# Optimization experiments

Measured on AMD Instinct MI355X. Metric: run time of the kernel, lower is better.

Reference implementation:

```python
import jax, jax.numpy as jnp
import numpy as np

B, C, W, H, D = 2, 256, 32, 32, 32
CH = C // 2  # 128
LN_EPS = 1e-5


def _spatial_pool(x, wm, bm):
    # x: [B,C,W,H,D]; wm: [C]; bm: scalar. 1x1x1 conv C->1 == channel dot.
    b, c = x.shape[0], x.shape[1]
    xf = x.reshape(b, c, -1)                       # [B,C,N]
    mask = jnp.einsum('bcn,c->bn', xf, wm) + bm    # [B,N]
    attn = jax.nn.softmax(mask, axis=1)            # softmax over spatial N
    return jnp.einsum('bcn,bn->bc', xf, attn)      # [B,C] weighted-sum pool


def _channel_add(ctx, w1, b1, g, be, w2, b2):
    # 1x1 conv C->C/2, LayerNorm over C/2, ReLU, 1x1 conv C/2->C
    h = ctx @ w1.T + b1                            # [B,CH]
    mu = jnp.mean(h, axis=-1, keepdims=True)
    var = jnp.mean((h - mu) ** 2, axis=-1, keepdims=True)
    h = (h - mu) * jax.lax.rsqrt(var + LN_EPS) * g + be
    h = jax.nn.relu(h)
    return h @ w2.T + b2                           # [B,C]


def setup_inputs() -> dict:
    key = jax.random.key(0)
    ks = jax.random.split(key, 20)
    s = 0.02
    d = {
        'preds_S': jax.random.normal(ks[0], (B, C, W, H, D), jnp.float32),
        'preds_T': jax.random.normal(ks[1], (B, C, W, H, D), jnp.float32),
        'wm_s': jax.random.normal(ks[2], (C,), jnp.float32) * s,
        'bm_s': jnp.zeros((), jnp.float32),
        'wm_t': jax.random.normal(ks[3], (C,), jnp.float32) * s,
        'bm_t': jnp.zeros((), jnp.float32),
        'w1_s': jax.random.normal(ks[4], (CH, C), jnp.float32) * s,
        'b1_s': jnp.zeros((CH,), jnp.float32),
        'g_s': jnp.ones((CH,), jnp.float32),
        'be_s': jnp.zeros((CH,), jnp.float32),
        'w2_s': jax.random.normal(ks[5], (C, CH), jnp.float32) * s,
        'b2_s': jnp.zeros((C,), jnp.float32),
        'w1_t': jax.random.normal(ks[6], (CH, C), jnp.float32) * s,
        'b1_t': jnp.zeros((CH,), jnp.float32),
        'g_t': jnp.ones((CH,), jnp.float32),
        'be_t': jnp.zeros((CH,), jnp.float32),
        'w2_t': jax.random.normal(ks[7], (C, CH), jnp.float32) * s,
        'b2_t': jnp.zeros((C,), jnp.float32),
    }
    return d


def reference(preds_S, preds_T, wm_s, bm_s, wm_t, bm_t,
              w1_s, b1_s, g_s, be_s, w2_s, b2_s,
              w1_t, b1_t, g_t, be_t, w2_t, b2_t):
    ctx_s = _spatial_pool(preds_S, wm_s, bm_s)     # [B,C]
    ctx_t = _spatial_pool(preds_T, wm_t, bm_t)
    add_s = _channel_add(ctx_s, w1_s, b1_s, g_s, be_s, w2_s, b2_s)  # [B,C]
    add_t = _channel_add(ctx_t, w1_t, b1_t, g_t, be_t, w2_t, b2_t)
    out_s = preds_S + add_s[:, :, None, None, None]
    out_t = preds_T + add_t[:, :, None, None, None]
    diff = out_s - out_t
    return jnp.sum(diff * diff) / preds_S.shape[0]
```

## Files before the change

kernel.cpp:

```cpp
#include <hip/hip_runtime.h>
#include <math.h>

#define Bc   2
#define Cc   256
#define Nn   32768
#define CHc  128
#define LN_EPS 1e-5f

#define TN    64
#define TPB   512
#define NQ    16
#define CG    32
#define CPG   8
#define GRIDX (Nn / TN)
#define NSLOT 16

__global__ __launch_bounds__(TPB, 2) void gc_fused(
    const float* __restrict__ S, const float* __restrict__ T,
    const float* __restrict__ wms, const float* __restrict__ bms,
    const float* __restrict__ wmt, const float* __restrict__ bmt,
    float* __restrict__ ctxnum,
    float* __restrict__ rowsum,
    float* __restrict__ den,
    float* __restrict__ sumsq) {
  const int b    = blockIdx.y;
  const int tid  = threadIdx.x;
  const int nq   = tid & (NQ - 1);
  const int cg   = tid >> 4;
  const int wv   = tid >> 6;
  const int lane = tid & 63;
  const int c0   = cg * CPG;
  const int n0   = blockIdx.x * TN + nq * 4;
  const int slot = blockIdx.x & (NSLOT - 1);

  __shared__ float4 mredw[2][8][NQ];
  __shared__ float  cred[Cc * 17];
  __shared__ float  sqred[8];
  __shared__ float  denred[2][NQ];

  const float bS = bms[0];
  const float bT = bmt[0];

  const float* Sp = S + ((size_t)b * Cc + c0) * Nn + n0;
  const float* Tp = T + ((size_t)b * Cc + c0) * Nn + n0;

  float4 s4[CPG], t4[CPG];
#pragma unroll
  for (int i = 0; i < CPG; ++i) s4[i] = *(const float4*)(Sp + (size_t)i * Nn);
#pragma unroll
  for (int i = 0; i < CPG; ++i) t4[i] = *(const float4*)(Tp + (size_t)i * Nn);

  float wS[CPG], wT[CPG];
#pragma unroll
  for (int i = 0; i < CPG; ++i) { wS[i] = wms[c0 + i]; wT[i] = wmt[c0 + i]; }

  float4 ms = make_float4(0.f, 0.f, 0.f, 0.f);
  float4 mt = make_float4(0.f, 0.f, 0.f, 0.f);
#pragma unroll
  for (int i = 0; i < CPG; ++i) {
    ms.x += wS[i] * s4[i].x; ms.y += wS[i] * s4[i].y;
    ms.z += wS[i] * s4[i].z; ms.w += wS[i] * s4[i].w;
    mt.x += wT[i] * t4[i].x; mt.y += wT[i] * t4[i].y;
    mt.z += wT[i] * t4[i].z; mt.w += wT[i] * t4[i].w;
  }

#pragma unroll
  for (int m = 16; m <= 32; m <<= 1) {
    ms.x += __shfl_xor(ms.x, m); ms.y += __shfl_xor(ms.y, m);
    ms.z += __shfl_xor(ms.z, m); ms.w += __shfl_xor(ms.w, m);
    mt.x += __shfl_xor(mt.x, m); mt.y += __shfl_xor(mt.y, m);
    mt.z += __shfl_xor(mt.z, m); mt.w += __shfl_xor(mt.w, m);
  }
  if (lane < NQ) { mredw[0][wv][nq] = ms; mredw[1][wv][nq] = mt; }

  __syncthreads();

  float4 Ms = make_float4(0.f, 0.f, 0.f, 0.f);
  float4 Mt = make_float4(0.f, 0.f, 0.f, 0.f);
#pragma unroll
  for (int w = 0; w < 8; ++w) {
    const float4 a = mredw[0][w][nq];
    Ms.x += a.x; Ms.y += a.y; Ms.z += a.z; Ms.w += a.w;
    const float4 c = mredw[1][w][nq];
    Mt.x += c.x; Mt.y += c.y; Mt.z += c.z; Mt.w += c.w;
  }
  float4 es, et;
  es.x = __expf(Ms.x + bS); es.y = __expf(Ms.y + bS);
  es.z = __expf(Ms.z + bS); es.w = __expf(Ms.w + bS);
  et.x = __expf(Mt.x + bT); et.y = __expf(Mt.y + bT);
  et.z = __expf(Mt.z + bT); et.w = __expf(Mt.w + bT);

  if (tid < NQ) {
    denred[0][tid] = es.x + es.y + es.z + es.w;
    denred[1][tid] = et.x + et.y + et.z + et.w;
  }

#pragma unroll
  for (int i = 0; i < CPG; ++i)
    cred[(c0 + i) * 17 + nq] =
        s4[i].x * es.x + s4[i].y * es.y + s4[i].z * es.z + s4[i].w * es.w;
  __syncthreads();
  if (tid < Cc) {
    float a = 0.f;
#pragma unroll
    for (int k = 0; k < NQ; ++k) a += cred[tid * 17 + k];
    atomicAdd(&ctxnum[(((size_t)slot * 2 + 0) * Bc + b) * Cc + tid], a);
  } else if (tid == Cc + 1) {
    float a = 0.f, c = 0.f;
#pragma unroll
    for (int k = 0; k < NQ; ++k) { a += denred[0][k]; c += denred[1][k]; }
    atomicAdd(&den[slot * 4 + 0 * Bc + b], a);
    atomicAdd(&den[slot * 4 + 1 * Bc + b], c);
  }
  __syncthreads();

#pragma unroll
  for (int i = 0; i < CPG; ++i)
    cred[(c0 + i) * 17 + nq] =
        t4[i].x * et.x + t4[i].y * et.y + t4[i].z * et.z + t4[i].w * et.w;
  __syncthreads();
  if (tid < Cc) {
    float c = 0.f;
#pragma unroll
    for (int k = 0; k < NQ; ++k) c += cred[tid * 17 + k];
    atomicAdd(&ctxnum[(((size_t)slot * 2 + 1) * Bc + b) * Cc + tid], c);
  }
  __syncthreads();

  float sq = 0.f;
#pragma unroll
  for (int i = 0; i < CPG; ++i) {
    const float dx = s4[i].x - t4[i].x, dy = s4[i].y - t4[i].y;
    const float dz = s4[i].z - t4[i].z, dw = s4[i].w - t4[i].w;
    cred[(c0 + i) * 17 + nq] = dx + dy + dz + dw;
    sq += dx * dx + dy * dy + dz * dz + dw * dw;
  }
#pragma unroll
  for (int m = 1; m < 64; m <<= 1) sq += __shfl_xor(sq, m);
  if (lane == 0) sqred[wv] = sq;
  __syncthreads();
  if (tid < Cc) {
    float r = 0.f;
#pragma unroll
    for (int k = 0; k < NQ; ++k) r += cred[tid * 17 + k];
    atomicAdd(&rowsum[((size_t)slot * Bc + b) * Cc + tid], r);
  } else if (tid == Cc) {
    float v = 0.f;
#pragma unroll
    for (int w = 0; w < 8; ++w) v += sqred[w];
    atomicAdd(&sumsq[slot], v);
  }
}

__global__ __launch_bounds__(1024) void gc_k4a_mlp(
    const float* __restrict__ ctxr, const float* __restrict__ den,
    const float* __restrict__ w1s, const float* __restrict__ b1s,
    const float* __restrict__ gs,  const float* __restrict__ bes,
    const float* __restrict__ w2s, const float* __restrict__ b2s,
    const float* __restrict__ w1t, const float* __restrict__ b1t,
    const float* __restrict__ gt,  const float* __restrict__ bet,
    const float* __restrict__ w2t, const float* __restrict__ b2t,
    float* __restrict__ addv) {
  const int tt  = blockIdx.x >> 1;
  const int b   = blockIdx.x & 1;
  const int tid = threadIdx.x;

  const float* w1 = tt ? w1t : w1s;
  const float* b1 = tt ? b1t : b1s;
  const float* g  = tt ? gt  : gs;
  const float* be = tt ? bet : bes;
  const float* w2 = tt ? w2t : w2s;
  const float* b2 = tt ? b2t : b2s;

  __shared__ float cxs[Cc];
  __shared__ float part[1024];
  __shared__ float hbuf[CHc];
  __shared__ float hr[CHc];
  __shared__ float2 red2[128];
  __shared__ float mu_s, rstd_s;

  if (tid < Cc) {
    float num = 0.f, dn = 0.f;
#pragma unroll
    for (int k = 0; k < NSLOT; ++k) {
      num += ctxr[(((size_t)k * 2 + tt) * Bc + b) * Cc + tid];
      dn  += den[k * 4 + tt * Bc + b];
    }
    cxs[tid] = num / dn;
  }
  __syncthreads();

  {
    const int j = tid >> 3, s = tid & 7;
    const float* wr = w1 + j * Cc + s * 32;
    const float4* cx4 = (const float4*)(cxs + s * 32);
    float acc = 0.f;
#pragma unroll
    for (int k = 0; k < 8; ++k) {
      const float4 w = *(const float4*)(wr + k * 4);
      const float4 x = cx4[k];
      acc += w.x * x.x + w.y * x.y + w.z * x.z + w.w * x.w;
    }
    part[tid] = acc;
  }
  __syncthreads();
  if (tid < CHc) {
    float h = b1[tid];
#pragma unroll
    for (int q = 0; q < 8; ++q) h += part[tid * 8 + q];
    hbuf[tid] = h;
  }
  __syncthreads();

  if (tid < CHc) {
    const float v = hbuf[tid];
    red2[tid] = make_float2(v, v * v);
  }
  __syncthreads();
  for (int s = 64; s > 0; s >>= 1) {
    if (tid < s) {
      red2[tid].x += red2[tid + s].x;
      red2[tid].y += red2[tid + s].y;
    }
    __syncthreads();
  }
  if (tid == 0) {
    const float mu = red2[0].x / (float)CHc;
    const float var = red2[0].y / (float)CHc - mu * mu;
    mu_s = mu;
    rstd_s = rsqrtf(var + LN_EPS);
  }
  __syncthreads();
  if (tid < CHc) {
    const float v = (hbuf[tid] - mu_s) * rstd_s * g[tid] + be[tid];
    hr[tid] = v > 0.f ? v : 0.f;
  }
  __syncthreads();

  {
    const int c = tid >> 2, q = tid & 3;
    const float* wr = w2 + c * CHc + q * 32;
    const float4* h4 = (const float4*)(hr + q * 32);
    float acc = 0.f;
#pragma unroll
    for (int k = 0; k < 8; ++k) {
      const float4 w = *(const float4*)(wr + k * 4);
      const float4 x = h4[k];
      acc += w.x * x.x + w.y * x.y + w.z * x.z + w.w * x.w;
    }
    part[tid] = acc;
  }
  __syncthreads();
  if (tid < Cc) {
    float acc = b2[tid];
#pragma unroll
    for (int q = 0; q < 4; ++q) acc += part[tid * 4 + q];
    addv[((size_t)tt * Bc + b) * Cc + tid] = acc;
  }
}

__global__ __launch_bounds__(256) void gc_k4b_final(
    const float* __restrict__ addv, const float* __restrict__ rowsum,
    const float* __restrict__ sumsq, float* __restrict__ out) {
  const int tid = threadIdx.x;
  __shared__ float red[256];
  float part = 0.f;
  for (int job = tid; job < Bc * Cc; job += 256) {
    const int c = job & (Cc - 1);
    const int b = job >> 8;
    const float delta = addv[((size_t)0 * Bc + b) * Cc + c] -
                        addv[((size_t)1 * Bc + b) * Cc + c];
    float rs = 0.f;
#pragma unroll
    for (int k = 0; k < NSLOT; ++k)
      rs += rowsum[((size_t)k * Bc + b) * Cc + c];
    part += 2.f * delta * rs + (float)Nn * delta * delta;
  }
  red[tid] = part;
  __syncthreads();
  for (int s = 128; s > 0; s >>= 1) {
    if (tid < s) red[tid] += red[tid + s];
    __syncthreads();
  }
  if (tid == 0) {
    float sq = 0.f;
#pragma unroll
    for (int k = 0; k < NSLOT; ++k) sq += sumsq[k];
    out[0] = (red[0] + sq) / (float)Bc;
  }
}

extern "C" void kernel_launch(void* const* d_in, const int* in_sizes, int n_in,
                              void* d_out, int out_size, void* d_ws,
                              size_t ws_size, hipStream_t stream) {
  const float* S   = (const float*)d_in[0];
  const float* T   = (const float*)d_in[1];
  const float* wms = (const float*)d_in[2];
  const float* bms = (const float*)d_in[3];
  const float* wmt = (const float*)d_in[4];
  const float* bmt = (const float*)d_in[5];
  const float* w1s = (const float*)d_in[6];
  const float* b1s = (const float*)d_in[7];
  const float* gs  = (const float*)d_in[8];
  const float* bes = (const float*)d_in[9];
  const float* w2s = (const float*)d_in[10];
  const float* b2s = (const float*)d_in[11];
  const float* w1t = (const float*)d_in[12];
  const float* b1t = (const float*)d_in[13];
  const float* gt  = (const float*)d_in[14];
  const float* bet = (const float*)d_in[15];
  const float* w2t = (const float*)d_in[16];
  const float* b2t = (const float*)d_in[17];
  float* out = (float*)d_out;

  float* ws     = (float*)d_ws;
  float* ctxnum = ws;
  float* rowsum = ctxnum + NSLOT * 2 * Bc * Cc;
  float* den    = rowsum + NSLOT * Bc * Cc;
  float* sumsq  = den + NSLOT * 4;
  float* addv   = sumsq + NSLOT;

  hipMemsetAsync(d_ws, 0,
                 (NSLOT * (2 * Bc * Cc + Bc * Cc + 4 + 1)) * sizeof(float),
                 stream);

  gc_fused<<<dim3(GRIDX, Bc), TPB, 0, stream>>>(S, T, wms, bms, wmt, bmt,
                                                ctxnum, rowsum, den, sumsq);
  gc_k4a_mlp<<<4, 1024, 0, stream>>>(ctxnum, den, w1s, b1s, gs, bes, w2s, b2s,
                                     w1t, b1t, gt, bet, w2t, b2t, addv);
  gc_k4b_final<<<1, 256, 0, stream>>>(addv, rowsum, sumsq, out);
}
```

Before: 195.8 us.

## Replace LDS channel reductions with wave shuffles and widen atomic slots

The per-channel partial sums for the student context, teacher context and S−T rowsum are now reduced with 16-lane xor shuffles in registers. Each lane then picks one channel's value and issues the global atomic itself, instead of staging through a padded shared-memory array. This removes the cred/denred shared buffers and several block-wide barriers, which should shorten the critical path and lower LDS use. The number of atomic slots is doubled to spread contention. The cost is more shuffle instructions and register pressure, and more slots for the MLP kernel to sum.

Result: no change. 192.6 us (-1.7%).

```diff
diff --git a/kernel.cpp b/kernel.cpp
--- a/kernel.cpp
+++ b/kernel.cpp
@@ -13,7 +13,7 @@
 #define CG    32
 #define CPG   8
 #define GRIDX (Nn / TN)
-#define NSLOT 16
+#define NSLOT 32
 
 __global__ __launch_bounds__(TPB, 2) void gc_fused(
     const float* __restrict__ S, const float* __restrict__ T,
@@ -29,14 +29,13 @@
   const int cg   = tid >> 4;
   const int wv   = tid >> 6;
   const int lane = tid & 63;
+  const int sub  = lane & 15;
   const int c0   = cg * CPG;
   const int n0   = blockIdx.x * TN + nq * 4;
   const int slot = blockIdx.x & (NSLOT - 1);
 
   __shared__ float4 mredw[2][8][NQ];
-  __shared__ float  cred[Cc * 17];
   __shared__ float  sqred[8];
-  __shared__ float  denred[2][NQ];
 
   const float bS = bms[0];
   const float bT = bmt[0];
@@ -73,6 +72,24 @@
   }
   if (lane < NQ) { mredw[0][wv][nq] = ms; mredw[1][wv][nq] = mt; }
 
+  float pd[CPG];
+  float sq = 0.f;
+#pragma unroll
+  for (int i = 0; i < CPG; ++i) {
+    const float dx = s4[i].x - t4[i].x, dy = s4[i].y - t4[i].y;
+    const float dz = s4[i].z - t4[i].z, dw = s4[i].w - t4[i].w;
+    pd[i] = dx + dy + dz + dw;
+    sq += dx * dx + dy * dy + dz * dz + dw * dw;
+  }
+#pragma unroll
+  for (int m = 1; m <= 8; m <<= 1) {
+#pragma unroll
+    for (int i = 0; i < CPG; ++i) pd[i] += __shfl_xor(pd[i], m);
+  }
+#pragma unroll
+  for (int m = 1; m < 64; m <<= 1) sq += __shfl_xor(sq, m);
+  if (lane == 0) sqred[wv] = sq;
+
   __syncthreads();
 
   float4 Ms = make_float4(0.f, 0.f, 0.f, 0.f);
@@ -90,61 +107,46 @@
   et.x = __expf(Mt.x + bT); et.y = __expf(Mt.y + bT);
   et.z = __expf(Mt.z + bT); et.w = __expf(Mt.w + bT);
 
-  if (tid < NQ) {
-    denred[0][tid] = es.x + es.y + es.z + es.w;
-    denred[1][tid] = et.x + et.y + et.z + et.w;
-  }
-
-#pragma unroll
-  for (int i = 0; i < CPG; ++i)
-    cred[(c0 + i) * 17 + nq] =
-        s4[i].x * es.x + s4[i].y * es.y + s4[i].z * es.z + s4[i].w * es.w;
-  __syncthreads();
-  if (tid < Cc) {
-    float a = 0.f;
-#pragma unroll
-    for (int k = 0; k < NQ; ++k) a += cred[tid * 17 + k];
-    atomicAdd(&ctxnum[(((size_t)slot * 2 + 0) * Bc + b) * Cc + tid], a);
-  } else if (tid == Cc + 1) {
-    float a = 0.f, c = 0.f;
-#pragma unroll
-    for (int k = 0; k < NQ; ++k) { a += denred[0][k]; c += denred[1][k]; }
-    atomicAdd(&den[slot * 4 + 0 * Bc + b], a);
-    atomicAdd(&den[slot * 4 + 1 * Bc + b], c);
-  }
-  __syncthreads();
-
-#pragma unroll
-  for (int i = 0; i < CPG; ++i)
-    cred[(c0 + i) * 17 + nq] =
-        t4[i].x * et.x + t4[i].y * et.y + t4[i].z * et.z + t4[i].w * et.w;
-  __syncthreads();
-  if (tid < Cc) {
-    float c = 0.f;
-#pragma unroll
-    for (int k = 0; k < NQ; ++k) c += cred[tid * 17 + k];
-    atomicAdd(&ctxnum[(((size_t)slot * 2 + 1) * Bc + b) * Cc + tid], c);
-  }
-  __syncthreads();
-
-  float sq = 0.f;
+  float dens = es.x + es.y + es.z + es.w;
+  float dent = et.x + et.y + et.z + et.w;
+  float ps[CPG], pt[CPG];
 #pragma unroll
   for (int i = 0; i < CPG; ++i) {
-    const float dx = s4[i].x - t4[i].x, dy = s4[i].y - t4[i].y;
-    const float dz = s4[i].z - t4[i].z, dw = s4[i].w - t4[i].w;
-    cred[(c0 + i) * 17 + nq] = dx + dy + dz + dw;
-    sq += dx * dx + dy * dy + dz * dz + dw * dw;
-  }
-#pragma unroll
-  for (int m = 1; m < 64; m <<= 1) sq += __shfl_xor(sq, m);
-  if (lane == 0) sqred[wv] = sq;
-  __syncthreads();
-  if (tid < Cc) {
-    float r = 0.f;
-#pragma unroll
-    for (int k = 0; k < NQ; ++k) r += cred[tid * 17 + k];
-    atomicAdd(&rowsum[((size_t)slot * Bc + b) * Cc + tid], r);
-  } else if (tid == Cc) {
+    ps[i] = s4[i].x * es.x + s4[i].y * es.y + s4[i].z * es.z + s4[i].w * es.w;
+    pt[i] = t4[i].x * et.x + t4[i].y * et.y + t4[i].z * et.z + t4[i].w * et.w;
+  }
+#pragma unroll
+  for (int m = 1; m <= 8; m <<= 1) {
+#pragma unroll
+    for (int i = 0; i < CPG; ++i) {
+      ps[i] += __shfl_xor(ps[i], m);
+      pt[i] += __shfl_xor(pt[i], m);
+    }
+    dens += __shfl_xor(dens, m);
+    dent += __shfl_xor(dent, m);
+  }
+
+  const int k = sub & 7;
+  float vs = ps[0], vt = pt[0], vd = pd[0];
+#pragma unroll
+  for (int i = 1; i < CPG; ++i) {
+    const bool m = (k == i);
+    vs = m ? ps[i] : vs;
+    vt = m ? pt[i] : vt;
+    vd = m ? pd[i] : vd;
+  }
+
+  if (sub < 8) {
+    atomicAdd(&ctxnum[(((size_t)slot * 2 + 0) * Bc + b) * Cc + c0 + k], vs);
+    atomicAdd(&rowsum[((size_t)slot * Bc + b) * Cc + c0 + k], vd);
+  } else {
+    atomicAdd(&ctxnum[(((size_t)slot * 2 + 1) * Bc + b) * Cc + c0 + k], vt);
+  }
+  if (tid == 0) {
+    atomicAdd(&den[slot * 4 + 0 * Bc + b], dens);
+    atomicAdd(&den[slot * 4 + 1 * Bc + b], dent);
+  }
+  if (tid == 64) {
     float v = 0.f;
 #pragma unroll
     for (int w = 0; w < 8; ++w) v += sqred[w];
@@ -182,9 +184,9 @@
   if (tid < Cc) {
     float num = 0.f, dn = 0.f;
 #pragma unroll
-    for (int k = 0; k < NSLOT; ++k) {
-      num += ctxr[(((size_t)k * 2 + tt) * Bc + b) * Cc + tid];
-      dn  += den[k * 4 + tt * Bc + b];
+    for (int kk = 0; kk < NSLOT; ++kk) {
+      num += ctxr[(((size_t)kk * 2 + tt) * Bc + b) * Cc + tid];
+      dn  += den[kk * 4 + tt * Bc + b];
     }
     cxs[tid] = num / dn;
   }
@@ -196,9 +198,9 @@
     const float4* cx4 = (const float4*)(cxs + s * 32);
     float acc = 0.f;
 #pragma unroll
-    for (int k = 0; k < 8; ++k) {
-      const float4 w = *(const float4*)(wr + k * 4);
-      const float4 x = cx4[k];
+    for (int kk = 0; kk < 8; ++kk) {
+      const float4 w = *(const float4*)(wr + kk * 4);
+      const float4 x = cx4[kk];
       acc += w.x * x.x + w.y * x.y + w.z * x.z + w.w * x.w;
     }
     part[tid] = acc;
@@ -243,9 +245,9 @@
     const float4* h4 = (const float4*)(hr + q * 32);
     float acc = 0.f;
 #pragma unroll
-    for (int k = 0; k < 8; ++k) {
-      const float4 w = *(const float4*)(wr + k * 4);
-      const float4 x = h4[k];
+    for (int kk = 0; kk < 8; ++kk) {
+      const float4 w = *(const float4*)(wr + kk * 4);
+      const float4 x = h4[kk];
       acc += w.x * x.x + w.y * x.y + w.z * x.z + w.w * x.w;
     }
     part[tid] = acc;
```

## Double per-block spatial tile and fuse MLP with final reduction kernel

Applied to the files above, without the earlier changes.

The fused pooling kernel now gives each thread 8 spatial points per channel instead of 4, halving the grid and the number of atomic flushes per element. The reduction slot count doubles to match. The two small tail kernels (MLP and final reduction) are merged into one 1024-thread block that handles all four (tensor, batch) groups at once, removing one launch and the addv round trip through global memory. Risks are higher register pressure in the main kernel, which holds twice as many float4s, and a single-block tail that now does serial 32-slot reductions.

After: 222.5 us. 1.14x slower.

```diff
diff --git a/kernel.cpp b/kernel.cpp
--- a/kernel.cpp
+++ b/kernel.cpp
@@ -7,13 +7,12 @@
 #define CHc  128
 #define LN_EPS 1e-5f
 
-#define TN    64
+#define TN    128
 #define TPB   512
 #define NQ    16
-#define CG    32
 #define CPG   8
 #define GRIDX (Nn / TN)
-#define NSLOT 16
+#define NSLOT 32
 
 __global__ __launch_bounds__(TPB, 2) void gc_fused(
     const float* __restrict__ S, const float* __restrict__ T,
@@ -30,10 +29,11 @@
   const int wv   = tid >> 6;
   const int lane = tid & 63;
   const int c0   = cg * CPG;
-  const int n0   = blockIdx.x * TN + nq * 4;
+  const int n0   = blockIdx.x * TN + nq * 8;
   const int slot = blockIdx.x & (NSLOT - 1);
 
-  __shared__ float4 mredw[2][8][NQ];
+  __shared__ float4 mredwA[2][8][NQ];
+  __shared__ float4 mredwB[2][8][NQ];
   __shared__ float  cred[Cc * 17];
   __shared__ float  sqred[8];
   __shared__ float  denred[2][NQ];
@@ -44,61 +44,93 @@
   const float* Sp = S + ((size_t)b * Cc + c0) * Nn + n0;
   const float* Tp = T + ((size_t)b * Cc + c0) * Nn + n0;
 
-  float4 s4[CPG], t4[CPG];
-#pragma unroll
-  for (int i = 0; i < CPG; ++i) s4[i] = *(const float4*)(Sp + (size_t)i * Nn);
-#pragma unroll
-  for (int i = 0; i < CPG; ++i) t4[i] = *(const float4*)(Tp + (size_t)i * Nn);
+  float4 sa[CPG], sb[CPG], ta[CPG], tb[CPG];
+#pragma unroll
+  for (int i = 0; i < CPG; ++i) {
+    sa[i] = *(const float4*)(Sp + (size_t)i * Nn);
+    sb[i] = *(const float4*)(Sp + (size_t)i * Nn + 4);
+  }
+#pragma unroll
+  for (int i = 0; i < CPG; ++i) {
+    ta[i] = *(const float4*)(Tp + (size_t)i * Nn);
+    tb[i] = *(const float4*)(Tp + (size_t)i * Nn + 4);
+  }
 
   float wS[CPG], wT[CPG];
 #pragma unroll
   for (int i = 0; i < CPG; ++i) { wS[i] = wms[c0 + i]; wT[i] = wmt[c0 + i]; }
 
-  float4 ms = make_float4(0.f, 0.f, 0.f, 0.f);
-  float4 mt = make_float4(0.f, 0.f, 0.f, 0.f);
+  float4 msa = make_float4(0.f, 0.f, 0.f, 0.f);
+  float4 msb = make_float4(0.f, 0.f, 0.f, 0.f);
+  float4 mta = make_float4(0.f, 0.f, 0.f, 0.f);
+  float4 mtb = make_float4(0.f, 0.f, 0.f, 0.f);
 #pragma unroll
   for (int i = 0; i < CPG; ++i) {
-    ms.x += wS[i] * s4[i].x; ms.y += wS[i] * s4[i].y;
-    ms.z += wS[i] * s4[i].z; ms.w += wS[i] * s4[i].w;
-    mt.x += wT[i] * t4[i].x; mt.y += wT[i] * t4[i].y;
-    mt.z += wT[i] * t4[i].z; mt.w += wT[i] * t4[i].w;
+    msa.x += wS[i] * sa[i].x; msa.y += wS[i] * sa[i].y;
+    msa.z += wS[i] * sa[i].z; msa.w += wS[i] * sa[i].w;
+    msb.x += wS[i] * sb[i].x; msb.y += wS[i] * sb[i].y;
+    msb.z += wS[i] * sb[i].z; msb.w += wS[i] * sb[i].w;
+    mta.x += wT[i] * ta[i].x; mta.y += wT[i] * ta[i].y;
+    mta.z += wT[i] * ta[i].z; mta.w += wT[i] * ta[i].w;
+    mtb.x += wT[i] * tb[i].x; mtb.y += wT[i] * tb[i].y;
+    mtb.z += wT[i] * tb[i].z; mtb.w += wT[i] * tb[i].w;
   }
 
 #pragma unroll
   for (int m = 16; m <= 32; m <<= 1) {
-    ms.x += __shfl_xor(ms.x, m); ms.y += __shfl_xor(ms.y, m);
-    ms.z += __shfl_xor(ms.z, m); ms.w += __shfl_xor(ms.w, m);
-    mt.x += __shfl_xor(mt.x, m); mt.y += __shfl_xor(mt.y, m);
-    mt.z += __shfl_xor(mt.z, m); mt.w += __shfl_xor(mt.w, m);
-  }
-  if (lane < NQ) { mredw[0][wv][nq] = ms; mredw[1][wv][nq] = mt; }
-
-  __syncthreads();
-
-  float4 Ms = make_float4(0.f, 0.f, 0.f, 0.f);
-  float4 Mt = make_float4(0.f, 0.f, 0.f, 0.f);
+    msa.x += __shfl_xor(msa.x, m); msa.y += __shfl_xor(msa.y, m);
+    msa.z += __shfl_xor(msa.z, m); msa.w += __shfl_xor(msa.w, m);
+    msb.x += __shfl_xor(msb.x, m); msb.y += __shfl_xor(msb.y, m);
+    msb.z += __shfl_xor(msb.z, m); msb.w += __shfl_xor(msb.w, m);
+    mta.x += __shfl_xor(mta.x, m); mta.y += __shfl_xor(mta.y, m);
+    mta.z += __shfl_xor(mta.z, m); mta.w += __shfl_xor(mta.w, m);
+    mtb.x += __shfl_xor(mtb.x, m); mtb.y += __shfl_xor(mtb.y, m);
+    mtb.z += __shfl_xor(mtb.z, m); mtb.w += __shfl_xor(mtb.w, m);
+  }
+  if (lane < NQ) {
+    mredwA[0][wv][nq] = msa; mredwA[1][wv][nq] = mta;
+    mredwB[0][wv][nq] = msb; mredwB[1][wv][nq] = mtb;
+  }
+
+  __syncthreads();
+
+  float4 Msa = make_float4(0.f, 0.f, 0.f, 0.f);
+  float4 Msb = make_float4(0.f, 0.f, 0.f, 0.f);
+  float4 Mta = make_float4(0.f, 0.f, 0.f, 0.f);
+  float4 Mtb = make_float4(0.f, 0.f, 0.f, 0.f);
 #pragma unroll
   for (int w = 0; w < 8; ++w) {
-    const float4 a = mredw[0][w][nq];
-    Ms.x += a.x; Ms.y += a.y; Ms.z += a.z; Ms.w += a.w;
-    const float4 c = mredw[1][w][nq];
-    Mt.x += c.x; Mt.y += c.y; Mt.z += c.z; Mt.w += c.w;
-  }
-  float4 es, et;
-  es.x = __expf(Ms.x + bS); es.y = __expf(Ms.y + bS);
-  es.z = __expf(Ms.z + bS); es.w = __expf(Ms.w + bS);
-  et.x = __expf(Mt.x + bT); et.y = __expf(Mt.y + bT);
-  et.z = __expf(Mt.z + bT); et.w = __expf(Mt.w + bT);
+    const float4 a0 = mredwA[0][w][nq];
+    Msa.x += a0.x; Msa.y += a0.y; Msa.z += a0.z; Msa.w += a0.w;
+    const float4 b0 = mredwB[0][w][nq];
+    Msb.x += b0.x; Msb.y += b0.y; Msb.z += b0.z; Msb.w += b0.w;
+    const float4 c1 = mredwA[1][w][nq];
+    Mta.x += c1.x; Mta.y += c1.y; Mta.z += c1.z; Mta.w += c1.w;
+    const float4 d1 = mredwB[1][w][nq];
+    Mtb.x += d1.x; Mtb.y += d1.y; Mtb.z += d1.z; Mtb.w += d1.w;
+  }
+  float4 esa, esb, eta, etb;
+  esa.x = __expf(Msa.x + bS); esa.y = __expf(Msa.y + bS);
+  esa.z = __expf(Msa.z + bS); esa.w = __expf(Msa.w + bS);
+  esb.x = __expf(Msb.x + bS); esb.y = __expf(Msb.y + bS);
+  esb.z = __expf(Msb.z + bS); esb.w = __expf(Msb.w + bS);
+  eta.x = __expf(Mta.x + bT); eta.y = __expf(Mta.y + bT);
+  eta.z = __expf(Mta.z + bT); eta.w = __expf(Mta.w + bT);
+  etb.x = __expf(Mtb.x + bT); etb.y = __expf(Mtb.y + bT);
+  etb.z = __expf(Mtb.z + bT); etb.w = __expf(Mtb.w + bT);
 
   if (tid < NQ) {
-    denred[0][tid] = es.x + es.y + es.z + es.w;
-    denred[1][tid] = et.x + et.y + et.z + et.w;
+    denred[0][tid] = esa.x + esa.y + esa.z + esa.w +
+                     esb.x + esb.y + esb.z + esb.w;
+    denred[1][tid] = eta.x + eta.y + eta.z + eta.w +
+                     etb.x + etb.y + etb.z + etb.w;
   }
 
 #pragma unroll
   for (int i = 0; i < CPG; ++i)
     cred[(c0 + i) * 17 + nq] =
-        s4[i].x * es.x + s4[i].y * es.y + s4[i].z * es.z + s4[i].w * es.w;
+        sa[i].x * esa.x + sa[i].y * esa.y + sa[i].z * esa.z + sa[i].w * esa.w +
+        sb[i].x * esb.x + sb[i].y * esb.y + sb[i].z * esb.z + sb[i].w * esb.w;
   __syncthreads();
   if (tid < Cc) {
     float a = 0.f;
@@ -117,7 +149,8 @@
 #pragma unroll
   for (int i = 0; i < CPG; ++i)
     cred[(c0 + i) * 17 + nq] =
-        t4[i].x * et.x + t4[i].y * et.y + t4[i].z * et.z + t4[i].w * et.w;
+        ta[i].x * eta.x + ta[i].y * eta.y + ta[i].z * eta.z + ta[i].w * eta.w +
+        tb[i].x * etb.x + tb[i].y * etb.y + tb[i].z * etb.z + tb[i].w * etb.w;
   __syncthreads();
   if (tid < Cc) {
     float c = 0.f;
@@ -130,10 +163,14 @@
   float sq = 0.f;
 #pragma unroll
   for (int i = 0; i < CPG; ++i) {
-    const float dx = s4[i].x - t4[i].x, dy = s4[i].y - t4[i].y;
-    const float dz = s4[i].z - t4[i].z, dw = s4[i].w - t4[i].w;
-    cred[(c0 + i) * 17 + nq] = dx + dy + dz + dw;
-    sq += dx * dx + dy * dy + dz * dz + dw * dw;
+    const float dxa = sa[i].x - ta[i].x, dya = sa[i].y - ta[i].y;
+    const float dza = sa[i].z - ta[i].z, dwa = sa[i].w - ta[i].w;
+    const float dxb = sb[i].x - tb[i].x, dyb = sb[i].y - tb[i].y;
+    const float dzb = sb[i].z - tb[i].z, dwb = sb[i].w - tb[i].w;
+    cred[(c0 + i) * 17 + nq] =
+        dxa + dya + dza + dwa + dxb + dyb + dzb + dwb;
+    sq += dxa * dxa + dya * dya + dza * dza + dwa * dwa +
+          dxb * dxb + dyb * dyb + dzb * dzb + dwb * dwb;
   }
 #pragma unroll
   for (int m = 1; m < 64; m <<= 1) sq += __shfl_xor(sq, m);
@@ -152,7 +189,7 @@
   }
 }
 
-__global__ __launch_bounds__(1024) void gc_k4a_mlp(
+__global__ __launch_bounds__(1024) void gc_k4(
     const float* __restrict__ ctxr, const float* __restrict__ den,
     const float* __restrict__ w1s, const float* __restrict__ b1s,
     const float* __restrict__ gs,  const float* __restrict__ bes,
@@ -160,10 +197,13 @@
     const float* __restrict__ w1t, const float* __restrict__ b1t,
     const float* __restrict__ gt,  const float* __restrict__ bet,
     const float* __restrict__ w2t, const float* __restrict__ b2t,
-    float* __restrict__ addv) {
-  const int tt  = blockIdx.x >> 1;
-  const int b   = blockIdx.x & 1;
-  const int tid = threadIdx.x;
+    const float* __restrict__ rowsum, const float* __restrict__ sumsq,
+    float* __restrict__ out) {
+  const int tid  = threadIdx.x;
+  const int grp  = tid >> 8;
+  const int tt   = grp >> 1;
+  const int b    = grp & 1;
+  const int gtid = tid & 255;
 
   const float* w1 = tt ? w1t : w1s;
   const float* b1 = tt ? b1t : b1s;
@@ -172,113 +212,102 @@
   const float* w2 = tt ? w2t : w2s;
   const float* b2 = tt ? b2t : b2s;
 
-  __shared__ float cxs[Cc];
-  __shared__ float part[1024];
-  __shared__ float hbuf[CHc];
-  __shared__ float hr[CHc];
-  __shared__ float2 red2[128];
-  __shared__ float mu_s, rstd_s;
-
-  if (tid < Cc) {
+  __shared__ float  cxs[4][Cc];
+  __shared__ float  part[4][256];
+  __shared__ float  hbuf[4][CHc];
+  __shared__ float  hr[4][CHc];
+  __shared__ float2 red2[4][64];
+  __shared__ float  mu_s[4], rstd_s[4];
+  __shared__ float  rsf[Bc * Cc];
+  __shared__ float  addv_l[4][Cc];
+  __shared__ float  red[512];
+
+  {
     float num = 0.f, dn = 0.f;
 #pragma unroll
     for (int k = 0; k < NSLOT; ++k) {
-      num += ctxr[(((size_t)k * 2 + tt) * Bc + b) * Cc + tid];
+      num += ctxr[(((size_t)k * 2 + tt) * Bc + b) * Cc + gtid];
       dn  += den[k * 4 + tt * Bc + b];
     }
-    cxs[tid] = num / dn;
+    cxs[grp][gtid] = num / dn;
+  }
+  if (tid < Bc * Cc) {
+    const int c = tid & (Cc - 1);
+    const int bb = tid >> 8;
+    float rs = 0.f;
+#pragma unroll
+    for (int k = 0; k < NSLOT; ++k)
+      rs += rowsum[((size_t)k * Bc + bb) * Cc + c];
+    rsf[tid] = rs;
   }
   __syncthreads();
 
   {
-    const int j = tid >> 3, s = tid & 7;
-    const float* wr = w1 + j * Cc + s * 32;
-    const float4* cx4 = (const float4*)(cxs + s * 32);
+    const int j = gtid >> 1, s = gtid & 1;
+    const float* wr = w1 + j * Cc + s * 128;
+    const float4* cx4 = (const float4*)(&cxs[grp][s * 128]);
     float acc = 0.f;
 #pragma unroll
-    for (int k = 0; k < 8; ++k) {
-      const float4 w = *(const float4*)(wr + k * 4);
-      const float4 x = cx4[k];
+    for (int kk = 0; kk < 32; ++kk) {
+      const float4 w = *(const float4*)(wr + kk * 4);
+      const float4 x = cx4[kk];
       acc += w.x * x.x + w.y * x.y + w.z * x.z + w.w * x.w;
     }
-    part[tid] = acc;
-  }
-  __syncthreads();
-  if (tid < CHc) {
-    float h = b1[tid];
-#pragma unroll
-    for (int q = 0; q < 8; ++q) h += part[tid * 8 + q];
-    hbuf[tid] = h;
-  }
-  __syncthreads();
-
-  if (tid < CHc) {
-    const float v = hbuf[tid];
-    red2[tid] = make_float2(v, v * v);
-  }
-  __syncthreads();
-  for (int s = 64; s > 0; s >>= 1) {
-    if (tid < s) {
-      red2[tid].x += red2[tid + s].x;
-      red2[tid].y += red2[tid + s].y;
+    part[grp][gtid] = acc;
+  }
+  __syncthreads();
+  if (gtid < CHc)
+    hbuf[grp][gtid] = b1[gtid] + part[grp][2 * gtid] + part[grp][2 * gtid + 1];
+  __syncthreads();
+
+  if (gtid < 64) {
+    const float v0 = hbuf[grp][gtid], v1 = hbuf[grp][gtid + 64];
+    red2[grp][gtid] = make_float2(v0 + v1, v0 * v0 + v1 * v1);
+  }
+  __syncthreads();
+  for (int s = 32; s > 0; s >>= 1) {
+    if (gtid < s) {
+      red2[grp][gtid].x += red2[grp][gtid + s].x;
+      red2[grp][gtid].y += red2[grp][gtid + s].y;
     }
     __syncthreads();
   }
-  if (tid == 0) {
-    const float mu = red2[0].x / (float)CHc;
-    const float var = red2[0].y / (float)CHc - mu * mu;
-    mu_s = mu;
-    rstd_s = rsqrtf(var + LN_EPS);
-  }
-  __syncthreads();
-  if (tid < CHc) {
-    const float v = (hbuf[tid] - mu_s) * rstd_s * g[tid] + be[tid];
-    hr[tid] = v > 0.f ? v : 0.f;
+  if (gtid == 0) {
+    const float mu = red2[grp][0].x / (float)CHc;
+    const float var = red2[grp][0].y / (float)CHc - mu * mu;
+    mu_s[grp] = mu;
+    rstd_s[grp] = rsqrtf(var + LN_EPS);
+  }
+  __syncthreads();
+  if (gtid < CHc) {
+    const float v =
+        (hbuf[grp][gtid] - mu_s[grp]) * rstd_s[grp] * g[gtid] + be[gtid];
+    hr[grp][gtid] = v > 0.f ? v : 0.f;
   }
   __syncthreads();
 
   {
-    const int c = tid >> 2, q = tid & 3;
-    const float* wr = w2 + c * CHc + q * 32;
-    const float4* h4 = (const float4*)(hr + q * 32);
-    float acc = 0.f;
-#pragma unroll
-    for (int k = 0; k < 8; ++k) {
-      const float4 w = *(const float4*)(wr + k * 4);
-      const float4 x = h4[k];
+    const float* wr = w2 + gtid * CHc;
+    const float4* h4 = (const float4*)(&hr[grp][0]);
+    float acc = b2[gtid];
+#pragma unroll
+    for (int kk = 0; kk < 32; ++kk) {
+      const float4 w = *(const float4*)(wr + kk * 4);
+      const float4 x = h4[kk];
       acc += w.x * x.x + w.y * x.y + w.z * x.z + w.w * x.w;
     }
-    part[tid] = acc;
-  }
-  __syncthreads();
-  if (tid < Cc) {
-    float acc = b2[tid];
-#pragma unroll
-    for (int q = 0; q < 4; ++q) acc += part[tid * 4 + q];
-    addv[((size_t)tt * Bc + b) * Cc + tid] = acc;
-  }
-}
-
-__global__ __launch_bounds__(256) void gc_k4b_final(
-    const float* __restrict__ addv, const float* __restrict__ rowsum,
-    const float* __restrict__ sumsq, float* __restrict__ out) {
-  const int tid = threadIdx.x;
-  __shared__ float red[256];
-  float part = 0.f;
-  for (int job = tid; job < Bc * Cc; job += 256) {
-    const int c = job & (Cc - 1);
-    const int b = job >> 8;
-    const float delta = addv[((size_t)0 * Bc + b) * Cc + c] -
-                        addv[((size_t)1 * Bc + b) * Cc + c];
-    float rs = 0.f;
-#pragma unroll
-    for (int k = 0; k < NSLOT; ++k)
-      rs += rowsum[((size_t)k * Bc + b) * Cc + c];
-    part += 2.f * delta * rs + (float)Nn * delta * delta;
-  }
-  red[tid] = part;
-  __syncthreads();
-  for (int s = 128; s > 0; s >>= 1) {
+    addv_l[grp][gtid] = acc;
+  }
+  __syncthreads();
+
+  if (tid < Bc * Cc) {
+    const int c = tid & (Cc - 1);
+    const int bb = tid >> 8;
+    const float delta = addv_l[0 + bb][c] - addv_l[2 + bb][c];
+    red[tid] = 2.f * delta * rsf[tid] + (float)Nn * delta * delta;
+  }
+  __syncthreads();
+  for (int s = 256; s > 0; s >>= 1) {
     if (tid < s) red[tid] += red[tid + s];
     __syncthreads();
   }
@@ -318,7 +347,6 @@
   float* rowsum = ctxnum + NSLOT * 2 * Bc * Cc;
   float* den    = rowsum + NSLOT * Bc * Cc;
   float* sumsq  = den + NSLOT * 4;
-  float* addv   = sumsq + NSLOT;
 
   hipMemsetAsync(d_ws, 0,
                  (NSLOT * (2 * Bc * Cc + Bc * Cc + 4 + 1)) * sizeof(float),
@@ -326,7 +354,7 @@
 
   gc_fused<<<dim3(GRIDX, Bc), TPB, 0, stream>>>(S, T, wms, bms, wmt, bmt,
                                                 ctxnum, rowsum, den, sumsq);
-  gc_k4a_mlp<<<4, 1024, 0, stream>>>(ctxnum, den, w1s, b1s, gs, bes, w2s, b2s,
-                                     w1t, b1t, gt, bet, w2t, b2t, addv);
-  gc_k4b_final<<<1, 256, 0, stream>>>(addv, rowsum, sumsq, out);
+  gc_k4<<<1, 1024, 0, stream>>>(ctxnum, den, w1s, b1s, gs, bes, w2s, b2s,
+                                w1t, b1t, gt, bet, w2t, b2t,
+                                rowsum, sumsq, out);
 }
```
